# Optimization experiments

Hardware: AMD Instinct MI355X
Metric: run time of the kernel (lower is better)

Reference implementation:

```python
import jax, jax.numpy as jnp
import numpy as np

E, R, D, H = 8, 16, 2048, 8192
B, S = 2, 2048
SCALING = 2.0  # lora_alpha / r = 32 / 16


def gelu_new(x):
    # HF ACT2FN['gelu_new'] (tanh approximation), matches Phi config
    c = np.sqrt(2.0 / np.pi).astype(np.float32)
    return 0.5 * x * (1.0 + jnp.tanh(c * (x + 0.044715 * x * x * x)))


def _moe_lora(x, onehot, A, Bm):
    # x: [T,Din], A: [E,R,Din], Bm: [E,Dout,R], onehot: [T,E]
    # per-token low-rank projection for every expert (R is tiny), mask to the
    # assigned expert, then contract (e,r) jointly -> single [T,E*R]@[E*R,Dout] GEMM
    z = jnp.einsum('td,erd->ter', x, A) * onehot[:, :, None]  # [T,E,R]
    return jnp.einsum('ter,ehr->th', z, Bm)                   # [T,Dout]


def setup_inputs() -> dict:
    key = jax.random.key(0)
    ks = jax.random.split(key, 10)
    inv = lambda n: np.float32(1.0 / np.sqrt(n))
    return {
        'hidden_states': jax.random.normal(ks[0], (B, S, D), jnp.float32),
        'expert_idx': jax.random.randint(ks[1], (B, S), 0, E),
        'W1': jax.random.normal(ks[2], (H, D), jnp.float32) * inv(D),
        'b1': jax.random.normal(ks[3], (H,), jnp.float32) * 0.02,
        'A1': jax.random.normal(ks[4], (E, R, D), jnp.float32) * inv(D),
        'B1': jax.random.normal(ks[5], (E, H, R), jnp.float32) * 0.02,
        'W2': jax.random.normal(ks[6], (D, H), jnp.float32) * inv(H),
        'b2': jax.random.normal(ks[7], (D,), jnp.float32) * 0.02,
        'A2': jax.random.normal(ks[8], (E, R, H), jnp.float32) * inv(H),
        'B2': jax.random.normal(ks[9], (E, D, R), jnp.float32) * 0.02,
    }


def reference(hidden_states, expert_idx, W1, b1, A1, B1, W2, b2, A2, B2):
    b, s, d = hidden_states.shape
    x = hidden_states.reshape(b * s, d)                       # [T,D]
    onehot = jax.nn.one_hot(expert_idx.reshape(-1), A1.shape[0], dtype=x.dtype)
    # expert fc1: shared base layer + per-expert LoRA + shared bias
    h1 = x @ W1.T + b1 + SCALING * _moe_lora(x, onehot, A1, B1)
    y = gelu_new(h1)                                          # [T,H]
    # expert fc2
    out = y @ W2.T + b2 + SCALING * _moe_lora(y, onehot, A2, B2)
    return out.reshape(b, s, d)
```

## Files before the change

kernel.cpp:

```cpp
#include <hip/hip_runtime.h>
#include <hip/hip_bf16.h>
#include <math.h>

typedef __bf16 bf16_t;
typedef __bf16 bf16x4_t __attribute__((ext_vector_type(4)));
typedef __bf16 bf16x8_t __attribute__((ext_vector_type(8)));
typedef float  f32x4    __attribute__((ext_vector_type(4)));
typedef const __attribute__((address_space(3))) char* lds_cp;

#define NE  8
#define NR  16
#define ND  2048
#define NH  8192
#define NT  4096
#define NER 128
#define NK1 (ND + NER)
#define NK2 (NH + NER)

static __device__ __forceinline__ float gelu_fast(float x) {
    const float c2 = 1.5957691216057308f;
    float u2 = c2 * (x + 0.044715f * x * x * x);
    return x / (1.0f + __expf(-u2));
}

static __device__ __forceinline__ void load16_to_lds(const bf16_t* g, bf16_t* l) {
    __builtin_amdgcn_global_load_lds(
        (__attribute__((address_space(1))) void*)(g),
        (__attribute__((address_space(3))) void*)(l),
        16, 0, 0);
}

template <int OFF>
static __device__ __forceinline__ bf16x8_t ds_read_b128_o(lds_cp p) {
    bf16x8_t r;
    asm volatile("ds_read_b128 %0, %1 offset:%2"
                 : "=v"(r) : "v"(p), "i"(OFF));
    return r;
}

__global__ __launch_bounds__(256) void conv_x(
    const float* __restrict__ x, bf16_t* __restrict__ Xa1)
{
    const int i  = blockIdx.x * 256 + threadIdx.x;
    const int row = i >> 8;
    const int c8  = i & 255;
    f32x4 v0 = *(const f32x4*)(x + (long)i * 8);
    f32x4 v1 = *(const f32x4*)(x + (long)i * 8 + 4);
    bf16x8_t o = {(bf16_t)v0[0], (bf16_t)v0[1], (bf16_t)v0[2], (bf16_t)v0[3],
                  (bf16_t)v1[0], (bf16_t)v1[1], (bf16_t)v1[2], (bf16_t)v1[3]};
    *(bf16x8_t*)(Xa1 + (long)row * NK1 + (c8 << 3)) = o;
}

__global__ __launch_bounds__(256) void prep_main(
    const float* __restrict__ W, bf16_t* __restrict__ Waug,
    int ld, int shift8, int total8)
{
    const int i = blockIdx.x * 256 + threadIdx.x;
    if (i >= total8) return;
    const int row = i >> shift8;
    const int c8  = i & ((1 << shift8) - 1);
    f32x4 v0 = *(const f32x4*)(W + (long)i * 8);
    f32x4 v1 = *(const f32x4*)(W + (long)i * 8 + 4);
    bf16x8_t o = {(bf16_t)v0[0], (bf16_t)v0[1], (bf16_t)v0[2], (bf16_t)v0[3],
                  (bf16_t)v1[0], (bf16_t)v1[1], (bf16_t)v1[2], (bf16_t)v1[3]};
    *(bf16x8_t*)(Waug + (long)row * ld + (c8 << 3)) = o;
}

__global__ __launch_bounds__(256) void prep_lora(
    const float* __restrict__ Bl, bf16_t* __restrict__ Waug,
    int nrows, int K0, int ld, int total)
{
    const int i = blockIdx.x * 256 + threadIdx.x;
    if (i >= total) return;
    const int row = i >> 7;
    const int c   = i & 127;
    const int e   = c >> 4;
    const int r   = c & 15;
    float v = Bl[((long)e * nrows + row) * NR + r];
    Waug[(long)row * ld + K0 + c] = (bf16_t)v;
}

template <int SPLITS, int LD>
__global__ __launch_bounds__(256) void zred(
    const float* __restrict__ zp, const int* __restrict__ eidx,
    bf16_t* __restrict__ dst)
{
    const int i = blockIdx.x * 256 + threadIdx.x;
    const int t = i >> 7;
    const int c = i & 127;
    float s = 0.f;
#pragma unroll
    for (int j = 0; j < SPLITS; ++j) s += zp[(long)j * NT * 128 + i];
    const int e = eidx[t];
    float v = ((c >> 4) == e) ? 2.0f * s : 0.f;
    dst[(long)t * LD + c] = (bf16_t)v;
}

template <int BM, int BN, int W, int WM, int WN,
          int K, int LDA, int LDB, int LDC, int MODE>
__global__ __launch_bounds__(W * 64) void gemm_bt(
    const bf16_t* __restrict__ A,  const bf16_t* __restrict__ Bt,
    const float* __restrict__ bias, void* __restrict__ Cout)
{
    constexpr int RW  = BM / WM;
    constexpr int CW  = BN / WN;
    constexpr int MT  = RW / 16;
    constexpr int NTn = CW / 16;
    constexpr int AI  = BM / 16 / W;
    constexpr int BI  = BN / 16 / W;

    __shared__ union {
        struct { bf16_t As[2 * BM * 32]; bf16_t Bs[2 * BN * 32]; } s;
        bf16_t Cs[64 * 264];
    } u;

    const int tid   = threadIdx.x;
    const int wave  = tid >> 6;
    const int lane  = tid & 63;
    const int col16 = lane & 15;
    const int q     = lane >> 4;
    const int wm    = wave % WM;
    const int wn    = wave / WM;

    const int  rowA0 = blockIdx.y * BM;
    const int  colB0 = (MODE == 3) ? 0 : blockIdx.x * BN;
    const long koff  = (MODE == 3) ? (long)blockIdx.x * K : 0;

    const int srow  = lane >> 2;
    const int skoff = (lane & 3) * 8;

    const bf16_t* Agp[AI][2];
    const bf16_t* Bgp[BI][2];
    bf16_t*       AsD[AI][2];
    bf16_t*       BsD[BI][2];
#pragma unroll
    for (int jj = 0; jj < AI; ++jj) {
        const int j = (wave + jj * W) * 16;
#pragma unroll
        for (int h = 0; h < 2; ++h) {
            Agp[jj][h] = A + (long)(rowA0 + j + srow) * LDA + koff + h * 32 + skoff;
            AsD[jj][h] = &u.s.As[(h * BM + j) * 32];
        }
    }
#pragma unroll
    for (int jj = 0; jj < BI; ++jj) {
        const int j = (wave + jj * W) * 16;
#pragma unroll
        for (int h = 0; h < 2; ++h) {
            Bgp[jj][h] = Bt + (long)(colB0 + j + srow) * LDB + koff + h * 32 + skoff;
            BsD[jj][h] = &u.s.Bs[(h * BN + j) * 32];
        }
    }

    const bf16_t* Ard = &u.s.As[(wm * RW + col16) * 32 + q * 8];
    const bf16_t* Brd = &u.s.Bs[(wn * CW + col16) * 32 + q * 8];

    f32x4 acc[MT][NTn];
#pragma unroll
    for (int i = 0; i < MT; ++i)
#pragma unroll
        for (int j = 0; j < NTn; ++j)
            acc[i][j] = (f32x4){0.f, 0.f, 0.f, 0.f};

    for (int it = 0; it < K / 64; ++it) {
#pragma unroll
        for (int jj = 0; jj < AI; ++jj)
#pragma unroll
            for (int h = 0; h < 2; ++h) {
                load16_to_lds(Agp[jj][h], AsD[jj][h]);
                Agp[jj][h] += 64;
            }
#pragma unroll
        for (int jj = 0; jj < BI; ++jj)
#pragma unroll
            for (int h = 0; h < 2; ++h) {
                load16_to_lds(Bgp[jj][h], BsD[jj][h]);
                Bgp[jj][h] += 64;
            }
        __syncthreads();

#pragma unroll
        for (int h = 0; h < 2; ++h) {
            bf16x8_t af[MT], bfr[NTn];
#pragma unroll
            for (int mt = 0; mt < MT; ++mt)
                af[mt] = *(const bf16x8_t*)(Ard + (h * BM + mt * 16) * 32);
#pragma unroll
            for (int nt = 0; nt < NTn; ++nt)
                bfr[nt] = *(const bf16x8_t*)(Brd + (h * BN + nt * 16) * 32);
#pragma unroll
            for (int mt = 0; mt < MT; ++mt)
#pragma unroll
                for (int nt = 0; nt < NTn; ++nt)
                    acc[mt][nt] = __builtin_amdgcn_mfma_f32_16x16x32_bf16(
                        af[mt], bfr[nt], acc[mt][nt], 0, 0, 0);
        }
        __syncthreads();
    }

    if (MODE == 3) {
        float* Cf = (float*)Cout + (long)blockIdx.x * NT * LDC;
#pragma unroll
        for (int nt = 0; nt < NTn; ++nt) {
            const int col = wn * CW + nt * 16 + col16;
#pragma unroll
            for (int mt = 0; mt < MT; ++mt) {
                const int row0 = rowA0 + wm * RW + mt * 16 + q * 4;
#pragma unroll
                for (int i = 0; i < 4; ++i)
                    Cf[(long)(row0 + i) * LDC + col] = acc[mt][nt][i];
            }
        }
    }
}


#define BARRIER8() do { __builtin_amdgcn_sched_barrier(0); \
    __builtin_amdgcn_s_barrier(); \
    __builtin_amdgcn_sched_barrier(0); } while (0)

#define WAITLG8() do { asm volatile("s_waitcnt lgkmcnt(0)" ::: "memory"); \
    __builtin_amdgcn_sched_barrier(0); } while (0)

template <int N>
static __device__ __forceinline__ void wait_vm() {
    static_assert(N == 0 || N == 4 || N == 6, "unsupported vmcnt");
    if constexpr (N == 0) asm volatile("s_waitcnt vmcnt(0)" ::: "memory");
    if constexpr (N == 4) asm volatile("s_waitcnt vmcnt(4)" ::: "memory");
    if constexpr (N == 6) asm volatile("s_waitcnt vmcnt(6)" ::: "memory");
}

#define STAGE_A8(TT, KH) do { \
    char* ld_ = smem + (((((TT) & 1) << 1) + (KH)) * ASLOT) + sdW; \
    const bf16_t* g_ = gA + (long)(TT) * 64 + (KH) * 32; \
    _Pragma("unroll") \
    for (int j_ = 0; j_ < LA; ++j_) \
        load16_to_lds(g_ + (long)j_ * 128 * LDA_, (bf16_t*)(ld_ + j_ * 8192)); \
} while (0)

#define STAGE_B8(TT, KH) do { \
    char* ld_ = smem + BOFF0 + (((((TT) & 1) << 1) + (KH)) * BSLOT) + sdW; \
    const bf16_t* g_ = gB + (long)(TT) * 64 + (KH) * 32; \
    _Pragma("unroll") \
    for (int j_ = 0; j_ < LB; ++j_) \
        load16_to_lds(g_ + (long)j_ * 128 * LDB_, (bf16_t*)(ld_ + j_ * 8192)); \
} while (0)

#define RD_A8(RP, KH, MH) do { \
    lds_cp p_ = sb3 + (((RP) * 2 + (KH)) * ASLOT) \
              + (wm * RW + (MH) * (RW / 2)) * 64 + rdoff; \
    af[0] = ds_read_b128_o<0>(p_); \
    af[1] = ds_read_b128_o<1024>(p_); \
    if constexpr (MT2 > 2) { \
        af[2] = ds_read_b128_o<2048>(p_); \
        af[3] = ds_read_b128_o<3072>(p_); \
    } \
} while (0)

#define RD_B8(RP, KH) do { \
    lds_cp p_ = sb3 + BOFF0 + (((RP) * 2 + (KH)) * BSLOT) \
              + (wn * CW) * 64 + rdoff; \
    bfr[0] = ds_read_b128_o<0>(p_); \
    bfr[1] = ds_read_b128_o<1024>(p_); \
    bfr[2] = ds_read_b128_o<2048>(p_); \
    bfr[3] = ds_read_b128_o<3072>(p_); \
} while (0)

#define MFMA_PH8(MH) do { \
    __builtin_amdgcn_s_setprio(1); \
    _Pragma("unroll") \
    for (int mt_ = 0; mt_ < MT2; ++mt_) \
        _Pragma("unroll") \
        for (int nt_ = 0; nt_ < NTn; ++nt_) \
            acc[(MH) * MT2 + mt_][nt_] = __builtin_amdgcn_mfma_f32_16x16x32_bf16( \
                af[mt_], bfr[nt_], acc[(MH) * MT2 + mt_][nt_], 0, 0, 0); \
    __builtin_amdgcn_s_setprio(0); \
} while (0)

#define TILE8(T_, ST_) do { \
    const int rp_ = (T_) & 1; \
     \
    RD_A8(rp_, 0, 0); RD_B8(rp_, 0); \
    if (ST_ >= 1) STAGE_A8((T_) + 1, 1); \
    BARRIER8(); WAITLG8(); MFMA_PH8(0); BARRIER8(); \
     \
    RD_A8(rp_, 0, 1); \
    if (ST_ == 2) STAGE_B8((T_) + 2, 0); \
    BARRIER8(); WAITLG8(); MFMA_PH8(1); BARRIER8(); \
     \
    RD_A8(rp_, 1, 0); RD_B8(rp_, 1); \
    if (ST_ == 2) STAGE_A8((T_) + 2, 0); \
    BARRIER8(); WAITLG8(); MFMA_PH8(0); BARRIER8(); \
     \
    RD_A8(rp_, 1, 1); \
    if (ST_ == 2) { STAGE_B8((T_) + 2, 1); wait_vm<NV>(); } \
    else if (ST_ == 1) { wait_vm<0>(); } \
    BARRIER8(); WAITLG8(); MFMA_PH8(1); BARRIER8(); \
} while (0)

template <int BN, int WM, int WN, int KT, int LDA_, int LDB_, int LDC_, int MODE>
__global__ __launch_bounds__(512, 2) void gemm8(
    const bf16_t* __restrict__ A, const bf16_t* __restrict__ Bt,
    const float* __restrict__ bias, void* __restrict__ Cout)
{
    constexpr int BM    = 256;
    constexpr int RW    = BM / WM;
    constexpr int CW    = BN / WN;
    constexpr int MT    = RW / 16;
    constexpr int MT2   = MT / 2;
    constexpr int NTn   = CW / 16;
    constexpr int LA    = 2;
    constexpr int LB    = BN / 128;
    constexpr int NV    = LA + 2 * LB;
    constexpr int NTIL  = KT / 64;
    static_assert(NTIL >= 3, "need >=3 K-tiles");
    constexpr int ASLOT = 16384;
    constexpr int BSLOT = BN * 64;
    constexpr int BOFF0 = 4 * ASLOT;
    constexpr int RING  = BOFF0 + 4 * BSLOT;
    constexpr int CSB   = 64 * 264 * 2;
    constexpr int SMEM  = (MODE == 0 && CSB > RING) ? CSB : RING;

    __shared__ __align__(16) char smem[SMEM];

    const int tid   = threadIdx.x;
    const int wave  = tid >> 6;
    const int lane  = tid & 63;
    const int col16 = lane & 15;
    const int q     = lane >> 4;
    const int wm    = wave % WM;
    const int wn    = wave / WM;

    const int rowA0 = blockIdx.y * BM;
    const int colB0 = blockIdx.x * BN;

    const int srow = tid >> 2;
    const int sseg = (tid & 3) ^ ((tid >> 3) & 3);
    const bf16_t* gA = A  + (long)(rowA0 + srow) * LDA_ + sseg * 8;
    const bf16_t* gB = Bt + (long)(colB0 + srow) * LDB_ + sseg * 8;
    const int sdW = wave << 10;

    const int rdoff = col16 * 64 + ((q ^ ((lane >> 1) & 3)) << 4);
    lds_cp sb3 = (lds_cp)smem;

    bf16x8_t af[MT2];
    bf16x8_t bfr[NTn];
    f32x4 acc[MT][NTn];
#pragma unroll
    for (int i = 0; i < MT; ++i)
#pragma unroll
        for (int j = 0; j < NTn; ++j)
            acc[i][j] = (f32x4){0.f, 0.f, 0.f, 0.f};

    STAGE_A8(0, 0); STAGE_B8(0, 0); STAGE_A8(0, 1); STAGE_B8(0, 1);
    STAGE_A8(1, 0); STAGE_B8(1, 0); STAGE_B8(1, 1);
    wait_vm<NV>();
    BARRIER8();

    for (int t = 0; t < NTIL - 2; ++t) TILE8(t, 2);
    TILE8(NTIL - 2, 1);
    TILE8(NTIL - 1, 0);

    if (MODE == 1) {
        float* Cf = (float*)Cout;
#pragma unroll
        for (int nt = 0; nt < NTn; ++nt) {
            const int col = colB0 + wn * CW + nt * 16 + col16;
            const float bv = bias[col];
#pragma unroll
            for (int mt = 0; mt < MT; ++mt) {
                const int row0 = rowA0 + wm * RW + mt * 16 + q * 4;
#pragma unroll
                for (int i = 0; i < 4; ++i)
                    Cf[(long)(row0 + i) * LDC_ + col] = acc[mt][nt][i] + bv;
            }
        }
    } else {
        bf16_t* Cb = (bf16_t*)Cout;
        bf16_t* Cs = (bf16_t*)smem;
#pragma unroll
        for (int ph = 0; ph < BM / 64; ++ph) {
            const int phwm = (ph * 64) / RW;
            const int mtb  = ((ph * 64) % RW) / 16;
            if (wm == phwm) {
#pragma unroll
                for (int nt = 0; nt < NTn; ++nt) {
                    const int c = wn * CW + nt * 16 + col16;
                    const float bv = bias[colB0 + c];
#pragma unroll
                    for (int mt = 0; mt < 4; ++mt) {
                        const int rl = mt * 16 + q * 4;
#pragma unroll
                        for (int i = 0; i < 4; ++i)
                            Cs[(rl + i) * 264 + c] =
                                (bf16_t)gelu_fast(acc[mtb + mt][nt][i] + bv);
                    }
                }
            }
            __syncthreads();
            {
                constexpr int CPR = BN / 32;
                const int r  = tid / CPR;
                const int c0 = (tid % CPR) * 32;
                const long gbase =
                    (long)(rowA0 + ph * 64 + r) * LDC_ + colB0 + c0;
#pragma unroll
                for (int ch = 0; ch < 4; ++ch) {
                    bf16x8_t v = *(const bf16x8_t*)&Cs[r * 264 + c0 + ch * 8];
                    *(bf16x8_t*)&Cb[gbase + ch * 8] = v;
                }
            }
            __syncthreads();
        }
    }
}

extern "C" void kernel_launch(void* const* d_in, const int* in_sizes, int n_in,
                              void* d_out, int out_size, void* d_ws, size_t ws_size,
                              hipStream_t stream)
{
    const float* x    = (const float*)d_in[0];
    const int*   eidx = (const int*)  d_in[1];
    const float* W1   = (const float*)d_in[2];
    const float* b1   = (const float*)d_in[3];
    const float* A1   = (const float*)d_in[4];
    const float* B1   = (const float*)d_in[5];
    const float* W2   = (const float*)d_in[6];
    const float* b2   = (const float*)d_in[7];
    const float* A2   = (const float*)d_in[8];
    const float* B2   = (const float*)d_in[9];
    float* out = (float*)d_out;

    char* ws = (char*)d_ws;
    bf16_t* Xaug2 = (bf16_t*)(ws);
    bf16_t* Xaug1 = (bf16_t*)(ws + 68157440L);
    bf16_t* W1aug = (bf16_t*)(ws + 85983232L);
    bf16_t* W2aug = (bf16_t*)(ws + 68157440L);
    bf16_t* A1b   = (bf16_t*)(ws + 104000000L);
    bf16_t* A2b   = (bf16_t*)(ws + 104857600L);
    float*  zp1   = (float*) (ws + 106954752L);
    float*  zp2   = (float*) (ws + 85983232L);

    conv_x<<<NT * ND / 8 / 256, 256, 0, stream>>>(x, Xaug1);
    prep_main<<<(NER * ND / 8) / 256, 256, 0, stream>>>(A1, A1b, ND, 8, NER * ND / 8);
    {
        dim3 g(4, NT / 128);
        gemm_bt<128, 128, 4, 2, 2, 512, NK1, ND, 128, 3><<<g, 256, 0, stream>>>(
            Xaug1, A1b, nullptr, (void*)zp1);
    }
    zred<4, NK1><<<NT * 128 / 256, 256, 0, stream>>>(zp1, eidx, Xaug1 + ND);
    prep_main<<<(NH * ND / 8) / 256, 256, 0, stream>>>(W1, W1aug, NK1, 8, NH * ND / 8);
    prep_lora<<<(NH * NER) / 256, 256, 0, stream>>>(B1, W1aug, NH, ND, NK1, NH * NER);
    {
        dim3 g(NH / 256, NT / 256);
        gemm8<256, 2, 4, NK1, NK1, NK1, NK2, 0><<<g, 512, 0, stream>>>(
            Xaug1, W1aug, b1, (void*)Xaug2);
    }

    prep_main<<<(NER * NH / 8) / 256, 256, 0, stream>>>(A2, A2b, NH, 10, NER * NH / 8);
    {
        dim3 g(8, NT / 128);
        gemm_bt<128, 128, 4, 2, 2, 1024, NK2, NH, 128, 3><<<g, 256, 0, stream>>>(
            Xaug2, A2b, nullptr, (void*)zp2);
    }
    zred<8, NK2><<<NT * 128 / 256, 256, 0, stream>>>(zp2, eidx, Xaug2 + NH);
    prep_main<<<(ND * NH / 8) / 256, 256, 0, stream>>>(W2, W2aug, NK2, 10, ND * NH / 8);
    prep_lora<<<(ND * NER) / 256, 256, 0, stream>>>(B2, W2aug, ND, NH, NK2, ND * NER);
    {
        dim3 g(ND / 128, NT / 256);
        gemm8<128, 4, 2, NK2, NK2, NK2, ND, 1><<<g, 512, 0, stream>>>(
            Xaug2, W2aug, b2, (void*)out);
    }
}
```

Before: 555.4 us.

## Double-buffer LDS fragment registers to overlap ds_reads with MFMA phases

Splits the A/B fragment registers into two sets and issues each phase's LDS reads one phase ahead, so the MFMAs of the current phase run while the next fragments are in flight. Full lgkmcnt(0) waits are replaced by partial waits, and the first fragments of the next K-tile are prefetched after the last-phase barrier. The aim is to hide LDS read latency that previously sat serially before each MFMA burst. The cost is more VGPRs under a 512-thread, 2-blocks-per-CU launch bound, which could cause spills, and the counter-based waits must exactly match the LDS-op ordering.

```diff
diff --git a/kernel.cpp b/kernel.cpp
--- a/kernel.cpp
+++ b/kernel.cpp
@@ -219,8 +219,11 @@
     __builtin_amdgcn_s_barrier(); \
     __builtin_amdgcn_sched_barrier(0); } while (0)
 
-#define WAITLG8() do { asm volatile("s_waitcnt lgkmcnt(0)" ::: "memory"); \
-    __builtin_amdgcn_sched_barrier(0); } while (0)
+template <int N>
+static __device__ __forceinline__ void wait_lg() {
+    asm volatile("s_waitcnt lgkmcnt(%0)" :: "i"(N) : "memory");
+    __builtin_amdgcn_sched_barrier(0);
+}
 
 template <int N>
 static __device__ __forceinline__ void wait_vm() {
@@ -246,56 +249,62 @@
         load16_to_lds(g_ + (long)j_ * 128 * LDB_, (bf16_t*)(ld_ + j_ * 8192)); \
 } while (0)
 
-#define RD_A8(RP, KH, MH) do { \
+#define RD_A_TO(DST, RP, KH, MH) do { \
     lds_cp p_ = sb3 + (((RP) * 2 + (KH)) * ASLOT) \
               + (wm * RW + (MH) * (RW / 2)) * 64 + rdoff; \
-    af[0] = ds_read_b128_o<0>(p_); \
-    af[1] = ds_read_b128_o<1024>(p_); \
+    DST[0] = ds_read_b128_o<0>(p_); \
+    DST[1] = ds_read_b128_o<1024>(p_); \
     if constexpr (MT2 > 2) { \
-        af[2] = ds_read_b128_o<2048>(p_); \
-        af[3] = ds_read_b128_o<3072>(p_); \
+        DST[2] = ds_read_b128_o<2048>(p_); \
+        DST[3] = ds_read_b128_o<3072>(p_); \
     } \
 } while (0)
 
-#define RD_B8(RP, KH) do { \
+#define RD_B_TO(DST, RP, KH) do { \
     lds_cp p_ = sb3 + BOFF0 + (((RP) * 2 + (KH)) * BSLOT) \
               + (wn * CW) * 64 + rdoff; \
-    bfr[0] = ds_read_b128_o<0>(p_); \
-    bfr[1] = ds_read_b128_o<1024>(p_); \
-    bfr[2] = ds_read_b128_o<2048>(p_); \
-    bfr[3] = ds_read_b128_o<3072>(p_); \
-} while (0)
-
-#define MFMA_PH8(MH) do { \
+    DST[0] = ds_read_b128_o<0>(p_); \
+    DST[1] = ds_read_b128_o<1024>(p_); \
+    DST[2] = ds_read_b128_o<2048>(p_); \
+    DST[3] = ds_read_b128_o<3072>(p_); \
+} while (0)
+
+#define MFMA_C(AF, BF, MH) do { \
     __builtin_amdgcn_s_setprio(1); \
     _Pragma("unroll") \
     for (int mt_ = 0; mt_ < MT2; ++mt_) \
         _Pragma("unroll") \
         for (int nt_ = 0; nt_ < NTn; ++nt_) \
             acc[(MH) * MT2 + mt_][nt_] = __builtin_amdgcn_mfma_f32_16x16x32_bf16( \
-                af[mt_], bfr[nt_], acc[(MH) * MT2 + mt_][nt_], 0, 0, 0); \
+                AF[mt_], BF[nt_], acc[(MH) * MT2 + mt_][nt_], 0, 0, 0); \
     __builtin_amdgcn_s_setprio(0); \
 } while (0)
 
 #define TILE8(T_, ST_) do { \
     const int rp_ = (T_) & 1; \
      \
-    RD_A8(rp_, 0, 0); RD_B8(rp_, 0); \
+    RD_A_TO(afY, rp_, 0, 1); \
     if (ST_ >= 1) STAGE_A8((T_) + 1, 1); \
-    BARRIER8(); WAITLG8(); MFMA_PH8(0); BARRIER8(); \
+    BARRIER8(); wait_lg<MT2>(); MFMA_C(afX, bf0, 0); BARRIER8(); \
      \
-    RD_A8(rp_, 0, 1); \
+    RD_A_TO(afX, rp_, 1, 0); RD_B_TO(bf1, rp_, 1); \
     if (ST_ == 2) STAGE_B8((T_) + 2, 0); \
-    BARRIER8(); WAITLG8(); MFMA_PH8(1); BARRIER8(); \
+    BARRIER8(); wait_lg<MT2 + NTn>(); MFMA_C(afY, bf0, 1); BARRIER8(); \
      \
-    RD_A8(rp_, 1, 0); RD_B8(rp_, 1); \
+    RD_A_TO(afY, rp_, 1, 1); \
     if (ST_ == 2) STAGE_A8((T_) + 2, 0); \
-    BARRIER8(); WAITLG8(); MFMA_PH8(0); BARRIER8(); \
+    BARRIER8(); wait_lg<MT2>(); MFMA_C(afX, bf1, 0); BARRIER8(); \
      \
-    RD_A8(rp_, 1, 1); \
     if (ST_ == 2) { STAGE_B8((T_) + 2, 1); wait_vm<NV>(); } \
     else if (ST_ == 1) { wait_vm<0>(); } \
-    BARRIER8(); WAITLG8(); MFMA_PH8(1); BARRIER8(); \
+    BARRIER8(); \
+    if (ST_ >= 1) { \
+        RD_A_TO(afX, rp_ ^ 1, 0, 0); RD_B_TO(bf0, rp_ ^ 1, 0); \
+        wait_lg<MT2 + NTn>(); \
+    } else { \
+        wait_lg<0>(); \
+    } \
+    MFMA_C(afY, bf1, 1); BARRIER8(); \
 } while (0)
 
 template <int BN, int WM, int WN, int KT, int LDA_, int LDB_, int LDC_, int MODE>
@@ -343,8 +352,8 @@
     const int rdoff = col16 * 64 + ((q ^ ((lane >> 1) & 3)) << 4);
     lds_cp sb3 = (lds_cp)smem;
 
-    bf16x8_t af[MT2];
-    bf16x8_t bfr[NTn];
+    bf16x8_t afX[MT2], afY[MT2];
+    bf16x8_t bf0[NTn], bf1[NTn];
     f32x4 acc[MT][NTn];
 #pragma unroll
     for (int i = 0; i < MT; ++i)
@@ -356,6 +365,7 @@
     STAGE_A8(1, 0); STAGE_B8(1, 0); STAGE_B8(1, 1);
     wait_vm<NV>();
     BARRIER8();
+    RD_A_TO(afX, 0, 0, 0); RD_B_TO(bf0, 0, 0);
 
     for (int t = 0; t < NTIL - 2; ++t) TILE8(t, 2);
     TILE8(NTIL - 2, 1);
```

Measured after the change: 556.5 us. About the same (+0.2%).
